# Kernel tuning notes

Measured on AMD Instinct MI355X. Metric: run time of the kernel, lower is better.

The kernel has to match this reference:

```python
import jax, jax.numpy as jnp
import numpy as np

N_NODES = 50000
N_EDGES = 400000
IN_DIM = 128
HID_DIM = 128
OUT_DIM = 128


def setup_inputs() -> dict:
    key = jax.random.key(0)
    k_x, k_e, k_w1, k_b1, k_w2, k_b2 = jax.random.split(key, 6)
    x = jax.random.normal(k_x, (N_NODES, IN_DIM), dtype=jnp.float32)
    edge_index = jax.random.randint(k_e, (2, N_EDGES), 0, N_NODES, dtype=jnp.int64)
    # nn.Linear-style params: W is [out, in], kaiming-uniform-ish init
    lim1 = 1.0 / np.sqrt(IN_DIM)
    lim2 = 1.0 / np.sqrt(HID_DIM)
    W1 = jax.random.uniform(k_w1, (HID_DIM, IN_DIM), jnp.float32, -lim1, lim1)
    b1 = jax.random.uniform(k_b1, (HID_DIM,), jnp.float32, -lim1, lim1)
    W2 = jax.random.uniform(k_w2, (OUT_DIM, HID_DIM), jnp.float32, -lim2, lim2)
    b2 = jax.random.uniform(k_b2, (OUT_DIM,), jnp.float32, -lim2, lim2)
    return {"x": x, "edge_index": edge_index, "W1": W1, "b1": b1, "W2": W2, "b2": b2}


def reference(x, edge_index, W1, b1, W2, b2):
    # h = relu(fc1(x));  dropout in eval mode -> identity
    h = jax.nn.relu(x @ W1.T + b1)                      # [N, hid]
    src, dst = edge_index[0], edge_index[1]
    # gather messages from src, scatter-add (mean) into dst
    agg = jax.ops.segment_sum(h[src], dst, num_segments=N_NODES)      # [N, hid]
    deg = jax.ops.segment_sum(jnp.ones_like(dst, dtype=h.dtype), dst,
                              num_segments=N_NODES)                   # [N]
    deg = jnp.maximum(deg, 1.0)
    agg = agg / deg[:, None]
    # residual add + fc2
    return (agg + h) @ W2.T + b2                        # [N, out]
```

## Files before the change

### kernel.cpp

```cpp
#include <hip/hip_runtime.h>

#define N_NODES 50000
#define N_EDGES 400000
#define DIM 128
#define N_SCAN_BLK ((N_NODES + 255) / 256)
#define BUCKET_BLK ((N_EDGES + 255) / 256)
#define FC1_BLK ((N_NODES + 63) / 64)

typedef unsigned short u16;
typedef unsigned int   u32;
typedef __bf16 v8bf  __attribute__((ext_vector_type(8)));
typedef float  f32x4 __attribute__((ext_vector_type(4)));
typedef u16    u16x8 __attribute__((ext_vector_type(8)));

union BF8 { u16x8 u; v8bf b; };

__device__ __forceinline__ float bf2f(u16 u) {
    union { u32 i; float f; } v; v.i = ((u32)u) << 16; return v.f;
}
__device__ __forceinline__ u16 f2bf(float f) {
    union { float f; u32 i; } v; v.f = f; u32 u = v.i;
    return (u16)((u + 0x7FFFu + ((u >> 16) & 1u)) >> 16);
}

__global__ __launch_bounds__(256) void count_cast_kernel(
    const int* __restrict__ edst, int* __restrict__ counts,
    const float* __restrict__ W1, const float* __restrict__ W2,
    u16* __restrict__ Wb1, u16* __restrict__ Wb2)
{
    int bid = blockIdx.x;
    if (bid < BUCKET_BLK) {
        int e = bid * 256 + threadIdx.x;
        if (e >= N_EDGES) return;
        int dst = edst[e];
        if ((unsigned)dst >= N_NODES) return;
        atomicAdd(&counts[dst], 1);
    } else {
        int i = (bid - BUCKET_BLK) * 256 + threadIdx.x;
        if (i < DIM * DIM) {
            Wb1[i] = f2bf(W1[i]);
            Wb2[i] = f2bf(W2[i]);
        }
    }
}

__global__ __launch_bounds__(256) void scan_blocks_kernel(
    const int* __restrict__ counts, int* __restrict__ row_ptr,
    int* __restrict__ bsum)
{
    __shared__ int tmp[256];
    const int t = threadIdx.x;
    const int i = blockIdx.x * 256 + t;
    int v = (i < N_NODES) ? counts[i] : 0;
    tmp[t] = v;
    __syncthreads();
#pragma unroll
    for (int ofs = 1; ofs < 256; ofs <<= 1) {
        int add = (t >= ofs) ? tmp[t - ofs] : 0;
        __syncthreads();
        tmp[t] += add;
        __syncthreads();
    }
    if (i < N_NODES) row_ptr[i] = tmp[t] - v;
    if (t == 255) bsum[blockIdx.x] = tmp[255];
}

__global__ __launch_bounds__(256) void scan_fixup2_kernel(
    const int* __restrict__ bsum, int* __restrict__ row_ptr,
    int* __restrict__ cursor)
{
    __shared__ int tmp[256];
    __shared__ int ex[256];
    const int t = threadIdx.x;
    int v = (t < N_SCAN_BLK) ? bsum[t] : 0;
    tmp[t] = v;
    __syncthreads();
#pragma unroll
    for (int ofs = 1; ofs < 256; ofs <<= 1) {
        int add = (t >= ofs) ? tmp[t - ofs] : 0;
        __syncthreads();
        tmp[t] += add;
        __syncthreads();
    }
    ex[t] = tmp[t] - v;
    __syncthreads();

    int boff = ex[blockIdx.x];
    int i = blockIdx.x * 256 + t;
    if (i < N_NODES) {
        int r = row_ptr[i] + boff;
        row_ptr[i] = r;
        cursor[i]  = r;
    }
    if (i == 0) row_ptr[N_NODES] = N_EDGES;
}

__global__ __launch_bounds__(256, 3) void bucket_fc1_kernel(
    const int* __restrict__ esrc, const int* __restrict__ edst,
    int* __restrict__ cursor, int* __restrict__ esorted,
    const float* __restrict__ x, const u16* __restrict__ Wb,
    const float* __restrict__ b, u16* __restrict__ h)
{
    __shared__ u16 xs[64 * 136];
    const int bid = blockIdx.x;

    if (bid < BUCKET_BLK) {
        int e = bid * 256 + threadIdx.x;
        if (e < N_EDGES) {
            int src = esrc[e], dst = edst[e];
            if ((unsigned)src < N_NODES && (unsigned)dst < N_NODES) {
                int pos = atomicAdd(&cursor[dst], 1);
                esorted[pos] = src;
            }
        }
        return;
    }

    const int t = threadIdx.x;
    const int wave = t >> 6, lane = t & 63, quad = lane >> 4, l15 = lane & 15;
    const int ch = wave >> 1, rh = wave & 1;
    const int row0 = (bid - BUCKET_BLK) * 64;

    BF8 barr[4][4];
#pragma unroll
    for (int ct = 0; ct < 4; ++ct)
#pragma unroll
        for (int ks = 0; ks < 4; ++ks)
            barr[ct][ks].u = *(const u16x8*)(
                Wb + (size_t)(ch * 64 + ct * 16 + l15) * DIM + ks * 32 + quad * 8);

    {
        int srow = t >> 2, k0 = (t & 3) * 32;
        int grow = row0 + srow; if (grow >= N_NODES) grow = N_NODES - 1;
        const float* xp = x + (size_t)grow * DIM + k0;
#pragma unroll
        for (int j = 0; j < 4; ++j) {
            float4 f0 = *(const float4*)(xp + j * 8);
            float4 f1 = *(const float4*)(xp + j * 8 + 4);
            u16x8 p;
            p[0] = f2bf(f0.x); p[1] = f2bf(f0.y); p[2] = f2bf(f0.z); p[3] = f2bf(f0.w);
            p[4] = f2bf(f1.x); p[5] = f2bf(f1.y); p[6] = f2bf(f1.z); p[7] = f2bf(f1.w);
            *(u16x8*)&xs[srow * 136 + k0 + j * 8] = p;
        }
    }

    f32x4 acc[2][4];
#pragma unroll
    for (int ct = 0; ct < 4; ++ct) {
        float bv = b[ch * 64 + ct * 16 + l15];
        acc[0][ct] = (f32x4){bv, bv, bv, bv};
        acc[1][ct] = (f32x4){bv, bv, bv, bv};
    }
    __syncthreads();

#pragma unroll
    for (int ks = 0; ks < 4; ++ks) {
        BF8 a0, a1;
        a0.u = *(const u16x8*)&xs[(rh * 32 +  0 + l15) * 136 + ks * 32 + quad * 8];
        a1.u = *(const u16x8*)&xs[(rh * 32 + 16 + l15) * 136 + ks * 32 + quad * 8];
#pragma unroll
        for (int ct = 0; ct < 4; ++ct) {
            acc[0][ct] = __builtin_amdgcn_mfma_f32_16x16x32_bf16(
                a0.b, barr[ct][ks].b, acc[0][ct], 0, 0, 0);
            acc[1][ct] = __builtin_amdgcn_mfma_f32_16x16x32_bf16(
                a1.b, barr[ct][ks].b, acc[1][ct], 0, 0, 0);
        }
    }

#pragma unroll
    for (int rt = 0; rt < 2; ++rt)
#pragma unroll
        for (int i = 0; i < 4; ++i) {
            int row = row0 + rh * 32 + rt * 16 + quad * 4 + i;
            if (row < N_NODES) {
#pragma unroll
                for (int ct = 0; ct < 4; ++ct) {
                    int col = ch * 64 + ct * 16 + l15;
                    h[(size_t)row * DIM + col] = f2bf(fmaxf(acc[rt][ct][i], 0.f));
                }
            }
        }
}

__global__ __launch_bounds__(256) void aggregate_kernel(
    const int* __restrict__ row_ptr, const int* __restrict__ esorted,
    const u16* __restrict__ h, u16* __restrict__ z)
{
    const int wave = threadIdx.x >> 6;
    const int lane = threadIdx.x & 63;
    const int n = blockIdx.x * 4 + wave;
    if (n >= N_NODES) return;

    const int start = row_ptr[n];
    const int end   = row_ptr[n + 1];

    float a0 = 0.f, a1 = 0.f;
    int e = start;
    for (; e + 8 <= end; e += 8) {
        int s0 = esorted[e + 0], s1 = esorted[e + 1];
        int s2 = esorted[e + 2], s3 = esorted[e + 3];
        int s4 = esorted[e + 4], s5 = esorted[e + 5];
        int s6 = esorted[e + 6], s7 = esorted[e + 7];
        u32 v0 = *(const u32*)(h + (size_t)s0 * DIM + lane * 2);
        u32 v1 = *(const u32*)(h + (size_t)s1 * DIM + lane * 2);
        u32 v2 = *(const u32*)(h + (size_t)s2 * DIM + lane * 2);
        u32 v3 = *(const u32*)(h + (size_t)s3 * DIM + lane * 2);
        u32 v4 = *(const u32*)(h + (size_t)s4 * DIM + lane * 2);
        u32 v5 = *(const u32*)(h + (size_t)s5 * DIM + lane * 2);
        u32 v6 = *(const u32*)(h + (size_t)s6 * DIM + lane * 2);
        u32 v7 = *(const u32*)(h + (size_t)s7 * DIM + lane * 2);
        a0 += bf2f((u16)v0); a1 += bf2f((u16)(v0 >> 16));
        a0 += bf2f((u16)v1); a1 += bf2f((u16)(v1 >> 16));
        a0 += bf2f((u16)v2); a1 += bf2f((u16)(v2 >> 16));
        a0 += bf2f((u16)v3); a1 += bf2f((u16)(v3 >> 16));
        a0 += bf2f((u16)v4); a1 += bf2f((u16)(v4 >> 16));
        a0 += bf2f((u16)v5); a1 += bf2f((u16)(v5 >> 16));
        a0 += bf2f((u16)v6); a1 += bf2f((u16)(v6 >> 16));
        a0 += bf2f((u16)v7); a1 += bf2f((u16)(v7 >> 16));
    }
    for (; e + 4 <= end; e += 4) {
        int s0 = esorted[e + 0], s1 = esorted[e + 1];
        int s2 = esorted[e + 2], s3 = esorted[e + 3];
        u32 v0 = *(const u32*)(h + (size_t)s0 * DIM + lane * 2);
        u32 v1 = *(const u32*)(h + (size_t)s1 * DIM + lane * 2);
        u32 v2 = *(const u32*)(h + (size_t)s2 * DIM + lane * 2);
        u32 v3 = *(const u32*)(h + (size_t)s3 * DIM + lane * 2);
        a0 += bf2f((u16)v0); a1 += bf2f((u16)(v0 >> 16));
        a0 += bf2f((u16)v1); a1 += bf2f((u16)(v1 >> 16));
        a0 += bf2f((u16)v2); a1 += bf2f((u16)(v2 >> 16));
        a0 += bf2f((u16)v3); a1 += bf2f((u16)(v3 >> 16));
    }
    for (; e < end; ++e) {
        u32 v = *(const u32*)(h + (size_t)esorted[e] * DIM + lane * 2);
        a0 += bf2f((u16)v); a1 += bf2f((u16)(v >> 16));
    }

    int deg = end - start;
    float inv = (deg > 0) ? 1.f / (float)deg : 1.f;
    u32 r = *(const u32*)(h + (size_t)n * DIM + lane * 2);
    float z0 = a0 * inv + bf2f((u16)r);
    float z1 = a1 * inv + bf2f((u16)(r >> 16));
    u32 p = (u32)f2bf(z0) | ((u32)f2bf(z1) << 16);
    *(u32*)(z + (size_t)n * DIM + lane * 2) = p;
}

__global__ __launch_bounds__(256, 3) void fc2_mfma(
    const u16* __restrict__ z, const u16* __restrict__ Wb,
    const float* __restrict__ b, float* __restrict__ out)
{
    __shared__ u16 xs[64 * 136];
    const int t = threadIdx.x;
    const int wave = t >> 6, lane = t & 63, quad = lane >> 4, l15 = lane & 15;
    const int ch = wave >> 1, rh = wave & 1;
    const int row0 = blockIdx.x * 64;

    BF8 barr[4][4];
#pragma unroll
    for (int ct = 0; ct < 4; ++ct)
#pragma unroll
        for (int ks = 0; ks < 4; ++ks)
            barr[ct][ks].u = *(const u16x8*)(
                Wb + (size_t)(ch * 64 + ct * 16 + l15) * DIM + ks * 32 + quad * 8);

    {
        int srow = t >> 1, k0 = (t & 1) * 64;
        int grow = row0 + srow; if (grow >= N_NODES) grow = N_NODES - 1;
        const u16* zp = z + (size_t)grow * DIM + k0;
#pragma unroll
        for (int j = 0; j < 8; ++j)
            *(u16x8*)&xs[srow * 136 + k0 + j * 8] = *(const u16x8*)(zp + j * 8);
    }

    f32x4 acc[2][4];
#pragma unroll
    for (int ct = 0; ct < 4; ++ct) {
        float bv = b[ch * 64 + ct * 16 + l15];
        acc[0][ct] = (f32x4){bv, bv, bv, bv};
        acc[1][ct] = (f32x4){bv, bv, bv, bv};
    }
    __syncthreads();

#pragma unroll
    for (int ks = 0; ks < 4; ++ks) {
        BF8 a0, a1;
        a0.u = *(const u16x8*)&xs[(rh * 32 +  0 + l15) * 136 + ks * 32 + quad * 8];
        a1.u = *(const u16x8*)&xs[(rh * 32 + 16 + l15) * 136 + ks * 32 + quad * 8];
#pragma unroll
        for (int ct = 0; ct < 4; ++ct) {
            acc[0][ct] = __builtin_amdgcn_mfma_f32_16x16x32_bf16(
                a0.b, barr[ct][ks].b, acc[0][ct], 0, 0, 0);
            acc[1][ct] = __builtin_amdgcn_mfma_f32_16x16x32_bf16(
                a1.b, barr[ct][ks].b, acc[1][ct], 0, 0, 0);
        }
    }

#pragma unroll
    for (int rt = 0; rt < 2; ++rt)
#pragma unroll
        for (int i = 0; i < 4; ++i) {
            int row = row0 + rh * 32 + rt * 16 + quad * 4 + i;
            if (row < N_NODES) {
#pragma unroll
                for (int ct = 0; ct < 4; ++ct) {
                    int col = ch * 64 + ct * 16 + l15;
                    out[(size_t)row * DIM + col] = acc[rt][ct][i];
                }
            }
        }
}

extern "C" void kernel_launch(void* const* d_in, const int* in_sizes, int n_in,
                              void* d_out, int out_size, void* d_ws, size_t ws_size,
                              hipStream_t stream)
{
    const float* x  = (const float*)d_in[0];
    const int*   ei = (const int*)d_in[1];
    const float* W1 = (const float*)d_in[2];
    const float* b1 = (const float*)d_in[3];
    const float* W2 = (const float*)d_in[4];
    const float* b2 = (const float*)d_in[5];
    float* out = (float*)d_out;

    const int* esrc = ei;
    const int* edst = ei + N_EDGES;

    char* ws = (char*)d_ws;
    size_t off = 0;
    u16* h        = (u16*)(ws + off); off += (size_t)N_NODES * DIM * 2;
    u16* z        = (u16*)(ws + off); off += (size_t)N_NODES * DIM * 2;
    u16* Wb1      = (u16*)(ws + off); off += (size_t)DIM * DIM * 2;
    u16* Wb2      = (u16*)(ws + off); off += (size_t)DIM * DIM * 2;
    int* counts   = (int*)(ws + off); off += (size_t)N_NODES * 4;
    int* row_ptr  = (int*)(ws + off); off += (size_t)(N_NODES + 1) * 4;
    int* cursor   = (int*)(ws + off); off += (size_t)N_NODES * 4;
    int* esorted  = (int*)(ws + off); off += (size_t)N_EDGES * 4;
    int* bsum     = (int*)(ws + off); off += (size_t)N_SCAN_BLK * 4;

    hipMemsetAsync(counts, 0, (size_t)N_NODES * 4, stream);
    count_cast_kernel<<<BUCKET_BLK + 64, 256, 0, stream>>>(
        edst, counts, W1, W2, Wb1, Wb2);
    scan_blocks_kernel<<<N_SCAN_BLK, 256, 0, stream>>>(counts, row_ptr, bsum);
    scan_fixup2_kernel<<<N_SCAN_BLK, 256, 0, stream>>>(bsum, row_ptr, cursor);
    bucket_fc1_kernel<<<BUCKET_BLK + FC1_BLK, 256, 0, stream>>>(
        esrc, edst, cursor, esorted, x, Wb1, b1, h);
    aggregate_kernel<<<(N_NODES + 3) / 4, 256, 0, stream>>>(
        row_ptr, esorted, h, z);
    fc2_mfma<<<(N_NODES + 63) / 64, 256, 0, stream>>>(z, Wb2, b2, out);
}
```

Before: 178.7 us.

## Fuse neighbor aggregation and fc2 into one kernel via shared-memory z tile

Merges the aggregate kernel and the fc2 MFMA kernel into a single 1024-thread kernel. Each of the 16 waves aggregates 4 node rows into an LDS tile, then the waves run the 64x128 GEMM from that tile. This removes the z intermediate's global write and read plus one launch. In exchange, each wave now handles 4 nodes in sequence, so gather latency is less well hidden, and the large blocks plus the barrier may reduce occupancy and load balance.

```diff
diff --git a/kernel.cpp b/kernel.cpp
--- a/kernel.cpp
+++ b/kernel.cpp
@@ -182,131 +182,111 @@
         }
 }
 
-__global__ __launch_bounds__(256) void aggregate_kernel(
+__global__ __launch_bounds__(1024) void agg_fc2_kernel(
     const int* __restrict__ row_ptr, const int* __restrict__ esorted,
-    const u16* __restrict__ h, u16* __restrict__ z)
-{
-    const int wave = threadIdx.x >> 6;
-    const int lane = threadIdx.x & 63;
-    const int n = blockIdx.x * 4 + wave;
-    if (n >= N_NODES) return;
-
-    const int start = row_ptr[n];
-    const int end   = row_ptr[n + 1];
-
-    float a0 = 0.f, a1 = 0.f;
-    int e = start;
-    for (; e + 8 <= end; e += 8) {
-        int s0 = esorted[e + 0], s1 = esorted[e + 1];
-        int s2 = esorted[e + 2], s3 = esorted[e + 3];
-        int s4 = esorted[e + 4], s5 = esorted[e + 5];
-        int s6 = esorted[e + 6], s7 = esorted[e + 7];
-        u32 v0 = *(const u32*)(h + (size_t)s0 * DIM + lane * 2);
-        u32 v1 = *(const u32*)(h + (size_t)s1 * DIM + lane * 2);
-        u32 v2 = *(const u32*)(h + (size_t)s2 * DIM + lane * 2);
-        u32 v3 = *(const u32*)(h + (size_t)s3 * DIM + lane * 2);
-        u32 v4 = *(const u32*)(h + (size_t)s4 * DIM + lane * 2);
-        u32 v5 = *(const u32*)(h + (size_t)s5 * DIM + lane * 2);
-        u32 v6 = *(const u32*)(h + (size_t)s6 * DIM + lane * 2);
-        u32 v7 = *(const u32*)(h + (size_t)s7 * DIM + lane * 2);
-        a0 += bf2f((u16)v0); a1 += bf2f((u16)(v0 >> 16));
-        a0 += bf2f((u16)v1); a1 += bf2f((u16)(v1 >> 16));
-        a0 += bf2f((u16)v2); a1 += bf2f((u16)(v2 >> 16));
-        a0 += bf2f((u16)v3); a1 += bf2f((u16)(v3 >> 16));
-        a0 += bf2f((u16)v4); a1 += bf2f((u16)(v4 >> 16));
-        a0 += bf2f((u16)v5); a1 += bf2f((u16)(v5 >> 16));
-        a0 += bf2f((u16)v6); a1 += bf2f((u16)(v6 >> 16));
-        a0 += bf2f((u16)v7); a1 += bf2f((u16)(v7 >> 16));
-    }
-    for (; e + 4 <= end; e += 4) {
-        int s0 = esorted[e + 0], s1 = esorted[e + 1];
-        int s2 = esorted[e + 2], s3 = esorted[e + 3];
-        u32 v0 = *(const u32*)(h + (size_t)s0 * DIM + lane * 2);
-        u32 v1 = *(const u32*)(h + (size_t)s1 * DIM + lane * 2);
-        u32 v2 = *(const u32*)(h + (size_t)s2 * DIM + lane * 2);
-        u32 v3 = *(const u32*)(h + (size_t)s3 * DIM + lane * 2);
-        a0 += bf2f((u16)v0); a1 += bf2f((u16)(v0 >> 16));
-        a0 += bf2f((u16)v1); a1 += bf2f((u16)(v1 >> 16));
-        a0 += bf2f((u16)v2); a1 += bf2f((u16)(v2 >> 16));
-        a0 += bf2f((u16)v3); a1 += bf2f((u16)(v3 >> 16));
-    }
-    for (; e < end; ++e) {
-        u32 v = *(const u32*)(h + (size_t)esorted[e] * DIM + lane * 2);
-        a0 += bf2f((u16)v); a1 += bf2f((u16)(v >> 16));
-    }
-
-    int deg = end - start;
-    float inv = (deg > 0) ? 1.f / (float)deg : 1.f;
-    u32 r = *(const u32*)(h + (size_t)n * DIM + lane * 2);
-    float z0 = a0 * inv + bf2f((u16)r);
-    float z1 = a1 * inv + bf2f((u16)(r >> 16));
-    u32 p = (u32)f2bf(z0) | ((u32)f2bf(z1) << 16);
-    *(u32*)(z + (size_t)n * DIM + lane * 2) = p;
-}
-
-__global__ __launch_bounds__(256, 3) void fc2_mfma(
-    const u16* __restrict__ z, const u16* __restrict__ Wb,
+    const u16* __restrict__ h, const u16* __restrict__ Wb,
     const float* __restrict__ b, float* __restrict__ out)
 {
-    __shared__ u16 xs[64 * 136];
+    __shared__ u16 zs[64 * 136];
     const int t = threadIdx.x;
     const int wave = t >> 6, lane = t & 63, quad = lane >> 4, l15 = lane & 15;
-    const int ch = wave >> 1, rh = wave & 1;
+    const int rt = wave & 3, cw = wave >> 2;
     const int row0 = blockIdx.x * 64;
 
-    BF8 barr[4][4];
-#pragma unroll
-    for (int ct = 0; ct < 4; ++ct)
+    BF8 barr[2][4];
+#pragma unroll
+    for (int ct = 0; ct < 2; ++ct)
 #pragma unroll
         for (int ks = 0; ks < 4; ++ks)
             barr[ct][ks].u = *(const u16x8*)(
-                Wb + (size_t)(ch * 64 + ct * 16 + l15) * DIM + ks * 32 + quad * 8);
-
-    {
-        int srow = t >> 1, k0 = (t & 1) * 64;
-        int grow = row0 + srow; if (grow >= N_NODES) grow = N_NODES - 1;
-        const u16* zp = z + (size_t)grow * DIM + k0;
-#pragma unroll
-        for (int j = 0; j < 8; ++j)
-            *(u16x8*)&xs[srow * 136 + k0 + j * 8] = *(const u16x8*)(zp + j * 8);
-    }
-
-    f32x4 acc[2][4];
-#pragma unroll
-    for (int ct = 0; ct < 4; ++ct) {
-        float bv = b[ch * 64 + ct * 16 + l15];
-        acc[0][ct] = (f32x4){bv, bv, bv, bv};
-        acc[1][ct] = (f32x4){bv, bv, bv, bv};
+                Wb + (size_t)(cw * 32 + ct * 16 + l15) * DIM + ks * 32 + quad * 8);
+
+    for (int i = 0; i < 4; ++i) {
+        int srow = wave * 4 + i;
+        int n = row0 + srow;
+        u32 p = 0;
+        if (n < N_NODES) {
+            const int start = row_ptr[n];
+            const int end   = row_ptr[n + 1];
+            float a0 = 0.f, a1 = 0.f;
+            int e = start;
+            for (; e + 8 <= end; e += 8) {
+                int s0 = esorted[e + 0], s1 = esorted[e + 1];
+                int s2 = esorted[e + 2], s3 = esorted[e + 3];
+                int s4 = esorted[e + 4], s5 = esorted[e + 5];
+                int s6 = esorted[e + 6], s7 = esorted[e + 7];
+                u32 v0 = *(const u32*)(h + (size_t)s0 * DIM + lane * 2);
+                u32 v1 = *(const u32*)(h + (size_t)s1 * DIM + lane * 2);
+                u32 v2 = *(const u32*)(h + (size_t)s2 * DIM + lane * 2);
+                u32 v3 = *(const u32*)(h + (size_t)s3 * DIM + lane * 2);
+                u32 v4 = *(const u32*)(h + (size_t)s4 * DIM + lane * 2);
+                u32 v5 = *(const u32*)(h + (size_t)s5 * DIM + lane * 2);
+                u32 v6 = *(const u32*)(h + (size_t)s6 * DIM + lane * 2);
+                u32 v7 = *(const u32*)(h + (size_t)s7 * DIM + lane * 2);
+                a0 += bf2f((u16)v0); a1 += bf2f((u16)(v0 >> 16));
+                a0 += bf2f((u16)v1); a1 += bf2f((u16)(v1 >> 16));
+                a0 += bf2f((u16)v2); a1 += bf2f((u16)(v2 >> 16));
+                a0 += bf2f((u16)v3); a1 += bf2f((u16)(v3 >> 16));
+                a0 += bf2f((u16)v4); a1 += bf2f((u16)(v4 >> 16));
+                a0 += bf2f((u16)v5); a1 += bf2f((u16)(v5 >> 16));
+                a0 += bf2f((u16)v6); a1 += bf2f((u16)(v6 >> 16));
+                a0 += bf2f((u16)v7); a1 += bf2f((u16)(v7 >> 16));
+            }
+            for (; e + 4 <= end; e += 4) {
+                int s0 = esorted[e + 0], s1 = esorted[e + 1];
+                int s2 = esorted[e + 2], s3 = esorted[e + 3];
+                u32 v0 = *(const u32*)(h + (size_t)s0 * DIM + lane * 2);
+                u32 v1 = *(const u32*)(h + (size_t)s1 * DIM + lane * 2);
+                u32 v2 = *(const u32*)(h + (size_t)s2 * DIM + lane * 2);
+                u32 v3 = *(const u32*)(h + (size_t)s3 * DIM + lane * 2);
+                a0 += bf2f((u16)v0); a1 += bf2f((u16)(v0 >> 16));
+                a0 += bf2f((u16)v1); a1 += bf2f((u16)(v1 >> 16));
+                a0 += bf2f((u16)v2); a1 += bf2f((u16)(v2 >> 16));
+                a0 += bf2f((u16)v3); a1 += bf2f((u16)(v3 >> 16));
+            }
+            for (; e < end; ++e) {
+                u32 v = *(const u32*)(h + (size_t)esorted[e] * DIM + lane * 2);
+                a0 += bf2f((u16)v); a1 += bf2f((u16)(v >> 16));
+            }
+            int deg = end - start;
+            float inv = (deg > 0) ? 1.f / (float)deg : 1.f;
+            u32 r = *(const u32*)(h + (size_t)n * DIM + lane * 2);
+            float z0 = a0 * inv + bf2f((u16)r);
+            float z1 = a1 * inv + bf2f((u16)(r >> 16));
+            p = (u32)f2bf(z0) | ((u32)f2bf(z1) << 16);
+        }
+        *(u32*)&zs[srow * 136 + lane * 2] = p;
+    }
+
+    f32x4 acc[2];
+#pragma unroll
+    for (int ct = 0; ct < 2; ++ct) {
+        float bv = b[cw * 32 + ct * 16 + l15];
+        acc[ct] = (f32x4){bv, bv, bv, bv};
     }
     __syncthreads();
 
 #pragma unroll
     for (int ks = 0; ks < 4; ++ks) {
-        BF8 a0, a1;
-        a0.u = *(const u16x8*)&xs[(rh * 32 +  0 + l15) * 136 + ks * 32 + quad * 8];
-        a1.u = *(const u16x8*)&xs[(rh * 32 + 16 + l15) * 136 + ks * 32 + quad * 8];
-#pragma unroll
-        for (int ct = 0; ct < 4; ++ct) {
-            acc[0][ct] = __builtin_amdgcn_mfma_f32_16x16x32_bf16(
-                a0.b, barr[ct][ks].b, acc[0][ct], 0, 0, 0);
-            acc[1][ct] = __builtin_amdgcn_mfma_f32_16x16x32_bf16(
-                a1.b, barr[ct][ks].b, acc[1][ct], 0, 0, 0);
-        }
-    }
-
-#pragma unroll
-    for (int rt = 0; rt < 2; ++rt)
-#pragma unroll
-        for (int i = 0; i < 4; ++i) {
-            int row = row0 + rh * 32 + rt * 16 + quad * 4 + i;
-            if (row < N_NODES) {
-#pragma unroll
-                for (int ct = 0; ct < 4; ++ct) {
-                    int col = ch * 64 + ct * 16 + l15;
-                    out[(size_t)row * DIM + col] = acc[rt][ct][i];
-                }
-            }
-        }
+        BF8 a;
+        a.u = *(const u16x8*)&zs[(rt * 16 + l15) * 136 + ks * 32 + quad * 8];
+#pragma unroll
+        for (int ct = 0; ct < 2; ++ct)
+            acc[ct] = __builtin_amdgcn_mfma_f32_16x16x32_bf16(
+                a.b, barr[ct][ks].b, acc[ct], 0, 0, 0);
+    }
+
+#pragma unroll
+    for (int i = 0; i < 4; ++i) {
+        int row = row0 + rt * 16 + quad * 4 + i;
+        if (row < N_NODES) {
+#pragma unroll
+            for (int ct = 0; ct < 2; ++ct) {
+                int col = cw * 32 + ct * 16 + l15;
+                out[(size_t)row * DIM + col] = acc[ct][i];
+            }
+        }
+    }
 }
 
 extern "C" void kernel_launch(void* const* d_in, const int* in_sizes, int n_in,
@@ -327,7 +307,6 @@
     char* ws = (char*)d_ws;
     size_t off = 0;
     u16* h        = (u16*)(ws + off); off += (size_t)N_NODES * DIM * 2;
-    u16* z        = (u16*)(ws + off); off += (size_t)N_NODES * DIM * 2;
     u16* Wb1      = (u16*)(ws + off); off += (size_t)DIM * DIM * 2;
     u16* Wb2      = (u16*)(ws + off); off += (size_t)DIM * DIM * 2;
     int* counts   = (int*)(ws + off); off += (size_t)N_NODES * 4;
@@ -343,7 +322,6 @@
     scan_fixup2_kernel<<<N_SCAN_BLK, 256, 0, stream>>>(bsum, row_ptr, cursor);
     bucket_fc1_kernel<<<BUCKET_BLK + FC1_BLK, 256, 0, stream>>>(
         esrc, edst, cursor, esorted, x, Wb1, b1, h);
-    aggregate_kernel<<<(N_NODES + 3) / 4, 256, 0, stream>>>(
-        row_ptr, esorted, h, z);
-    fc2_mfma<<<(N_NODES + 63) / 64, 256, 0, stream>>>(z, Wb2, b2, out);
-}
+    agg_fc2_kernel<<<FC1_BLK, 1024, 0, stream>>>(
+        row_ptr, esorted, h, Wb2, b2, out);
+}
```

Result: slower. 196.2 us (+9.8%).
